# Optimization experiments

Measured on AMD Instinct MI355X. Metric: run time of the kernel, lower is better.

Reference implementation:

```python
import jax, jax.numpy as jnp
import numpy as np

N, E, MUL, ATTR, NBASIS = 30000, 480000, 32, 8, 8
AVG_NEIGH = 16.0
INV_SQRT3 = 1.0 / np.sqrt(3.0).astype(np.float32)  # wigner 3j (1,1,0)
LOG2 = float(np.log(2.0))


def ssp(x):
    # shifted softplus: softplus(x) - log(2)
    return jax.nn.softplus(x) - LOG2


def setup_inputs() -> dict:
    key = jax.random.key(0)
    ks = jax.random.split(key, 15)
    return {
        "node_s": jax.random.normal(ks[0], (N, MUL), jnp.float32),
        "node_v": jax.random.normal(ks[1], (N, MUL, 3), jnp.float32),
        "node_attr": jax.random.uniform(ks[2], (N, ATTR), jnp.float32),
        "edge_attr": jax.random.normal(ks[3], (E, 4), jnp.float32),       # [sh0 | sh1(3)]
        "edge_scalars": jax.random.uniform(ks[4], (E, NBASIS), jnp.float32),
        "W1_0": jax.random.normal(ks[5], (MUL, MUL), jnp.float32),
        "W1_1": jax.random.normal(ks[6], (MUL, MUL), jnp.float32),
        "Wfc1": jax.random.normal(ks[7], (NBASIS, NBASIS), jnp.float32),
        "Wfc2": jax.random.normal(ks[8], (NBASIS, 4 * MUL), jnp.float32),
        "W2_0": jax.random.normal(ks[9], (2 * MUL, MUL), jnp.float32),
        "W2_1": jax.random.normal(ks[10], (2 * MUL, MUL), jnp.float32),
        "Wsc0": jax.random.normal(ks[11], (MUL, ATTR, MUL), jnp.float32),
        "Wsc1": jax.random.normal(ks[12], (MUL, ATTR, MUL), jnp.float32),
        "edge_src": jax.random.randint(ks[13], (E,), 0, N, jnp.int32),
        "edge_dst": jax.random.randint(ks[14], (E,), 0, N, jnp.int32),
    }


def reference(node_s, node_v, node_attr, edge_attr, edge_scalars,
              W1_0, W1_1, Wfc1, Wfc2, W2_0, W2_1, Wsc0, Wsc1,
              edge_src, edge_dst):
    n_nodes, mul = node_s.shape
    # --- fc: radial MLP -> per-edge TP weights (shared_weights=False) ---
    h = ssp(edge_scalars @ Wfc1 * (1.0 / np.sqrt(Wfc1.shape[0])))
    w = h @ Wfc2 * (1.0 / np.sqrt(Wfc2.shape[0]))                 # [E, 4*MUL]
    w00, w01, w10, w11 = jnp.split(w, 4, axis=1)                  # instruction order
    # --- lin1: per-irrep linear (fan-in normalized) ---
    inv_m = 1.0 / np.sqrt(mul)
    x0 = node_s @ W1_0 * inv_m                                    # [N, MUL]
    x1 = jnp.einsum('nud,uw->nwd', node_v, W1_1) * inv_m          # [N, MUL, 3]
    # --- gather destination-node features per edge ---
    x0d, x1d = x0[edge_dst], x1[edge_dst]
    sh0, sh1 = edge_attr[:, :1], edge_attr[:, 1:4]
    # --- uvu tensor product with per-edge weights ---
    s_a = w00 * x0d * sh0                                         # 0e x 0e -> 0e
    s_b = w11 * jnp.einsum('eud,ed->eu', x1d, sh1) * INV_SQRT3    # 1o x 1o -> 0e
    v_a = (w01 * x0d)[:, :, None] * sh1[:, None, :]               # 0e x 1o -> 1o
    v_b = w10[:, :, None] * x1d * sh0[:, :, None]                 # 1o x 0e -> 1o
    mid_s = jnp.concatenate([s_a, s_b], axis=1)                   # [E, 64]  (64x0e)
    mid_v = jnp.concatenate([v_a, v_b], axis=1)                   # [E, 64, 3] (64x1o)
    # --- scatter-sum over edge_src, normalized by sqrt(avg_num_neighbors) ---
    inv_nb = 1.0 / np.sqrt(AVG_NEIGH)
    agg_s = jax.ops.segment_sum(mid_s, edge_src, num_segments=n_nodes) * inv_nb
    agg_v = jax.ops.segment_sum(mid_v, edge_src, num_segments=n_nodes) * inv_nb
    # --- lin2 ---
    inv_2m = 1.0 / np.sqrt(2.0 * mul)
    out0 = agg_s @ W2_0 * inv_2m                                  # [N, MUL]
    out1 = jnp.einsum('nud,uw->nwd', agg_v, W2_1) * inv_2m        # [N, MUL, 3]
    # --- self-connection: fully-connected TP (attr is scalar 8x0e) ---
    sc_norm = 1.0 / np.sqrt(mul * node_attr.shape[1])
    sc0 = jnp.einsum('nu,nv,uvw->nw', node_s, node_attr, Wsc0) * sc_norm
    sc1 = jnp.einsum('nud,nv,uvw->nwd', node_v, node_attr, Wsc1) * sc_norm
    o0 = out0 + sc0
    o1 = out1 + sc1
    return jnp.concatenate([o0, o1.reshape(n_nodes, mul * 3)], axis=1)  # [N, 128]
```

## Files before the change

### kernel.cpp

```cpp
#include <hip/hip_runtime.h>
#include <math.h>

#define N_NODES 30000
#define N_EDGES 480000

typedef __attribute__((ext_vector_type(8))) short short8;
typedef __attribute__((ext_vector_type(4))) float f32x4;
typedef __attribute__((ext_vector_type(2))) float f32x2;

__device__ __forceinline__ unsigned short f2bf(float f) {
    unsigned u = __float_as_uint(f);
    u += 0x7fff + ((u >> 16) & 1);
    return (unsigned short)(u >> 16);
}
__device__ __forceinline__ float bfLO(unsigned v) { return __uint_as_float(v << 16); }
__device__ __forceinline__ float bfHI(unsigned v) { return __uint_as_float(v & 0xffff0000u); }
__device__ __forceinline__ unsigned packbf(float a, float b) {
    return (unsigned)f2bf(a) | ((unsigned)f2bf(b) << 16);
}
__device__ __forceinline__ unsigned ptk(float a, float b) {
    return (__float_as_uint(a) >> 16) | (__float_as_uint(b) & 0xffff0000u);
}

union U8 { short8 v; unsigned u[4]; };
union C4 { f32x4 v; float f[4]; };

__global__ __launch_bounds__(256) void k_pre(
    const float* __restrict__ node_s,
    const float* __restrict__ node_v,
    const float* __restrict__ W1_0,
    const float* __restrict__ W1_1,
    const float* __restrict__ Wsc0,
    const float* __restrict__ Wsc1,
    const float* __restrict__ W2_0,
    const float* __restrict__ W2_1,
    const int* __restrict__ edge_src,
    int* __restrict__ deg,
    unsigned short* __restrict__ xnode,
    unsigned* __restrict__ bsc0,
    unsigned* __restrict__ bsc1,
    unsigned* __restrict__ b20,
    unsigned* __restrict__ b21)
{
    __shared__ float sVT[16 * 100];
    __shared__ float sXo[16 * 140];
    int tid = threadIdx.x;

    if (blockIdx.x >= 1875) {
        int b = blockIdx.x - 1875;
        const float* Wm = (b == 0) ? Wsc0 : (b == 1) ? Wsc1 : (b == 2) ? W2_0 : W2_1;
        unsigned* dst = (b == 0) ? bsc0 : (b == 1) ? bsc1 : (b == 2) ? b20 : b21;
        float scale = (b < 2) ? 0.0625f : 0.03125f;
        int nu = (b < 2) ? 4096 : 1024;
        for (int idx = tid; idx < nu; idx += 256) {
            int jp = idx & 3;
            int lane = (idx >> 2) & 63;
            int ft = (idx >> 8) & 1;
            int kc = idx >> 9;
            int quad = lane >> 4, col = lane & 15;
            int k = kc * 32 + quad * 8 + jp * 2;
            int c = ft * 16 + col;
            dst[idx] = packbf(Wm[k * 32 + c] * scale, Wm[(k + 1) * 32 + c] * scale);
        }
        return;
    }

    atomicAdd(&deg[edge_src[blockIdx.x * 256 + tid]], 1);

    int nbase = blockIdx.x * 16;
    for (int i = tid; i < 1536; i += 256) {
        int nl = i / 96, r = i - nl * 96;
        int u = r / 3, d = r - u * 3;
        sVT[nl * 100 + d * 32 + u] = node_v[(size_t)nbase * 96 + i];
    }
    __syncthreads();

    int lane = tid & 63;
    int wv = tid >> 6;
    int col = lane & 15, quad = lane >> 4, m = lane & 15;

    const float* W1 = (wv == 0) ? W1_0 : W1_1;
    U8 bf0, bf1;
#pragma unroll
    for (int p = 0; p < 4; ++p) {
        int k = quad * 8 + 2 * p;
        bf0.u[p] = packbf(W1[k * 32 + col],      W1[(k + 1) * 32 + col]);
        bf1.u[p] = packbf(W1[k * 32 + col + 16], W1[(k + 1) * 32 + col + 16]);
    }

    U8 af;
    if (wv == 0) {
        const float* sp = node_s + (size_t)(nbase + m) * 32 + quad * 8;
        float4 a0 = *(const float4*)(sp);
        float4 a1 = *(const float4*)(sp + 4);
        af.u[0] = packbf(a0.x, a0.y); af.u[1] = packbf(a0.z, a0.w);
        af.u[2] = packbf(a1.x, a1.y); af.u[3] = packbf(a1.z, a1.w);
    } else {
        int R = 16 * (wv - 1) + m;
        int nl = R / 3, d = R - nl * 3;
        const float* vp = sVT + nl * 100 + d * 32 + quad * 8;
        af.u[0] = packbf(vp[0], vp[1]); af.u[1] = packbf(vp[2], vp[3]);
        af.u[2] = packbf(vp[4], vp[5]); af.u[3] = packbf(vp[6], vp[7]);
    }

    f32x4 acc0 = {0.f, 0.f, 0.f, 0.f};
    f32x4 acc1 = {0.f, 0.f, 0.f, 0.f};
    acc0 = __builtin_amdgcn_mfma_f32_16x16x32_bf16(af.v, bf0.v, acc0, 0, 0, 0);
    acc1 = __builtin_amdgcn_mfma_f32_16x16x32_bf16(af.v, bf1.v, acc1, 0, 0, 0);

    C4 c0, c1;
    c0.v = acc0; c1.v = acc1;
    if (wv == 0) {
#pragma unroll
        for (int r = 0; r < 4; ++r) {
            int nl = (quad << 2) + r;
            sXo[nl * 140 + col]      = c0.f[r];
            sXo[nl * 140 + col + 16] = c1.f[r];
        }
    } else {
#pragma unroll
        for (int r = 0; r < 4; ++r) {
            int R = 16 * (wv - 1) + (quad << 2) + r;
            int nl = R / 3, d = R - nl * 3;
            sXo[nl * 140 + (1 + d) * 34 + col]      = c0.f[r];
            sXo[nl * 140 + (1 + d) * 34 + col + 16] = c1.f[r];
        }
    }
    __syncthreads();

    const float inv_m = 0.1767766953f;
    for (int i = tid; i < 512; i += 256) {
        int nl = i >> 5, u = i & 31;
        const float* xp = sXo + nl * 140;
        uint2 pk;
        pk.x = packbf(xp[u] * inv_m,       xp[34 + u] * inv_m);
        pk.y = packbf(xp[68 + u] * inv_m,  xp[102 + u] * inv_m);
        *(uint2*)(xnode + (size_t)(nbase + nl) * 128 + u * 4) = pk;
    }
}

__global__ __launch_bounds__(1024) void scan_kernel(const int* __restrict__ deg,
                                                    int* __restrict__ offs,
                                                    int* __restrict__ cursor) {
    __shared__ int sdeg[N_NODES];
    __shared__ int wsum[16];
    int tid = threadIdx.x;
#pragma unroll
    for (int k = 0; k < 30; ++k) {
        int idx = k * 1024 + tid;
        if (idx < N_NODES) sdeg[idx] = deg[idx];
    }
    __syncthreads();
    int base = tid * 30;
    int s = 0;
    if (base < N_NODES) {
#pragma unroll
        for (int k = 0; k < 30; ++k) s += sdeg[base + k];
    }
    int lane = tid & 63, wid = tid >> 6;
    int inc = s;
#pragma unroll
    for (int d = 1; d < 64; d <<= 1) {
        int o = __shfl_up(inc, d, 64);
        if (lane >= d) inc += o;
    }
    if (lane == 63) wsum[wid] = inc;
    __syncthreads();
    if (tid < 16) {
        int v = wsum[tid];
        int t = v;
#pragma unroll
        for (int d = 1; d < 16; d <<= 1) {
            int o = __shfl_up(t, d, 64);
            if (tid >= d) t += o;
        }
        wsum[tid] = t - v;
    }
    __syncthreads();
    int run = inc - s + wsum[wid];
    if (base < N_NODES) {
#pragma unroll
        for (int k = 0; k < 30; ++k) {
            int n = base + k;
            int d = sdeg[n];
            sdeg[n] = run;
            run += d;
        }
    }
    __syncthreads();
#pragma unroll
    for (int k = 0; k < 30; ++k) {
        int idx = k * 1024 + tid;
        if (idx < N_NODES) {
            int v = sdeg[idx];
            offs[idx] = v;
            cursor[idx] = v;
        }
    }
    if (tid == 0) offs[N_NODES] = N_EDGES;
}

__global__ __launch_bounds__(256) void fill_kernel(
    const float* __restrict__ edge_attr,
    const float* __restrict__ edge_scalars,
    const float* __restrict__ Wfc1,
    const int* __restrict__ edge_src,
    const int* __restrict__ edge_dst,
    int* __restrict__ cursor,
    uint4* __restrict__ rec)
{
    __shared__ float sW[64];
    int tid = threadIdx.x;
    if (tid < 64) sW[tid] = Wfc1[tid];
    __syncthreads();

    int e = blockIdx.x * 256 + tid;
    float4 es0 = *(const float4*)(edge_scalars + (size_t)e * 8);
    float4 es1 = *(const float4*)(edge_scalars + (size_t)e * 8 + 4);
    float4 ea  = *(const float4*)(edge_attr + (size_t)e * 4);
    int src = edge_src[e];
    int dst = edge_dst[e];
    int pos = atomicAdd(&cursor[src], 1);

    const float inv8 = 0.3535533906f;
    float h[8];
#pragma unroll
    for (int i = 0; i < 8; ++i) {
        float acc = es0.x * sW[0 * 8 + i];
        acc = fmaf(es0.y, sW[1 * 8 + i], acc);
        acc = fmaf(es0.z, sW[2 * 8 + i], acc);
        acc = fmaf(es0.w, sW[3 * 8 + i], acc);
        acc = fmaf(es1.x, sW[4 * 8 + i], acc);
        acc = fmaf(es1.y, sW[5 * 8 + i], acc);
        acc = fmaf(es1.z, sW[6 * 8 + i], acc);
        acc = fmaf(es1.w, sW[7 * 8 + i], acc);
        acc *= inv8;
        float ax = fabsf(acc);
        float tt = __expf(-ax);
        h[i] = fmaxf(acc, 0.f) + __logf(1.f + tt) - 0.6931471806f;
    }
    uint4 r0, r1;
    r0.x = packbf(h[0], h[1]); r0.y = packbf(h[2], h[3]);
    r0.z = packbf(h[4], h[5]); r0.w = packbf(h[6], h[7]);
    r1.x = packbf(ea.x, ea.y); r1.y = packbf(ea.z, ea.w);
    r1.z = ((unsigned)dst) << 8;
    r1.w = 0;
    rec[2 * pos]     = r0;
    rec[2 * pos + 1] = r1;
}

struct GAcc {
    float sa, sb, va2, vb2;
    f32x2 va01, vb01;
};

__device__ __forceinline__ void gstep(
    uint4& RS0, uint4& RS1, uint2& XS, const uint4& RN1, uint2& XN,
    int& t, int cntH, int& pf, int L,
    const char* recc, const char* xbc,
    const f32x2* wfA, const f32x2* wfB, GAcc& g)
{
    float hv[8];
    hv[0] = bfLO(RS0.x); hv[1] = bfHI(RS0.x);
    hv[2] = bfLO(RS0.y); hv[3] = bfHI(RS0.y);
    hv[4] = bfLO(RS0.z); hv[5] = bfHI(RS0.z);
    hv[6] = bfLO(RS0.w); hv[7] = bfHI(RS0.w);
    float sh0  = bfLO(RS1.x), s1xe = bfHI(RS1.x);
    float s1ye = bfLO(RS1.y), s1ze = bfHI(RS1.y);
    float xv0 = bfLO(XS.x), xd0 = bfHI(XS.x);
    float xd1 = bfLO(XS.y), xd2 = bfHI(XS.y);
    bool ok = (t < cntH);

    RS0 = *(const uint4*)(recc + pf);
    RS1 = *(const uint4*)(recc + pf + 16);
    pf = min(pf + 64, L);
    XN = *(const uint2*)(xbc + RN1.z);

    f32x2 aA = {0.f, 0.f}, aB = {0.f, 0.f};
#pragma unroll
    for (int q = 0; q < 8; ++q) {
        f32x2 hh = {hv[q], hv[q]};
        aA = __builtin_elementwise_fma(hh, wfA[q], aA);
        aB = __builtin_elementwise_fma(hh, wfB[q], aB);
    }
    float a00 = ok ? aA.x : 0.f;
    float a01 = ok ? aA.y : 0.f;
    float a10 = ok ? aB.x : 0.f;
    float a11 = ok ? aB.y : 0.f;

    float dot = xd0 * s1xe + xd1 * s1ye + xd2 * s1ze;
    g.sa = fmaf(a00 * sh0, xv0, g.sa);
    g.sb = fmaf(a11, dot, g.sb);
    float w01x0 = a01 * xv0;
    float t10 = a10 * sh0;
    f32x2 wb = {w01x0, w01x0};
    f32x2 tb = {t10, t10};
    f32x2 s01 = {s1xe, s1ye};
    f32x2 xd01 = {xd0, xd1};
    g.va01 = __builtin_elementwise_fma(wb, s01, g.va01);
    g.vb01 = __builtin_elementwise_fma(tb, xd01, g.vb01);
    g.va2 = fmaf(w01x0, s1ze, g.va2);
    g.vb2 = fmaf(t10, xd2, g.vb2);
    ++t;
}

__global__ __launch_bounds__(256) void k_gather(
    const int* __restrict__ offs,
    const uint4* __restrict__ rec,
    const float* __restrict__ Wfc2,
    const unsigned short* __restrict__ xnode,
    unsigned short* __restrict__ agg)
{
    int tid = threadIdx.x;
    int lane = tid & 63;
    int u = lane & 31;
    int half = lane >> 5;
    int wv = tid >> 6;
    int node = blockIdx.x * 4 + wv;

    const float inv8 = 0.3535533906f;
    const float i8s3 = 0.3535533906f * 0.5773502692f;
    f32x2 wfA[8], wfB[8];
#pragma unroll
    for (int q = 0; q < 8; ++q) {
        const float* wp = Wfc2 + q * 128 + u;
        wfA[q].x = wp[0]  * inv8;
        wfA[q].y = wp[32] * inv8;
        wfB[q].x = wp[64] * inv8;
        wfB[q].y = wp[96] * i8s3;
    }

    int beg = offs[node], end = offs[node + 1];
    int cnt = end - beg;

    GAcc g;
    g.sa = 0.f; g.sb = 0.f; g.va2 = 0.f; g.vb2 = 0.f;
    g.va01 = (f32x2){0.f, 0.f};
    g.vb01 = (f32x2){0.f, 0.f};

    if (cnt > 0) {
        const char* recc = (const char*)rec;
        const char* xbc  = (const char*)xnode + u * 8;
        int T = (cnt + 1) >> 1;
        int cntH = (cnt + 1 - half) >> 1;
        int L = (end - 1) * 32;
        int b0 = (beg + half) * 32;

        uint4 r00, r01, r10, r11, r20, r21, r30, r31, r40, r41, r50, r51;
        uint2 x0, x1, x2, x3, x4, x5;
        x4.x = 0u; x4.y = 0u; x5.x = 0u; x5.y = 0u;
        int p;
        p = min(b0,       L); r00 = *(const uint4*)(recc + p); r01 = *(const uint4*)(recc + p + 16);
        p = min(b0 + 64,  L); r10 = *(const uint4*)(recc + p); r11 = *(const uint4*)(recc + p + 16);
        p = min(b0 + 128, L); r20 = *(const uint4*)(recc + p); r21 = *(const uint4*)(recc + p + 16);
        p = min(b0 + 192, L); r30 = *(const uint4*)(recc + p); r31 = *(const uint4*)(recc + p + 16);
        p = min(b0 + 256, L); r40 = *(const uint4*)(recc + p); r41 = *(const uint4*)(recc + p + 16);
        p = min(b0 + 320, L); r50 = *(const uint4*)(recc + p); r51 = *(const uint4*)(recc + p + 16);
        int pf = min(b0 + 384, L);
        x0 = *(const uint2*)(xbc + r01.z);
        x1 = *(const uint2*)(xbc + r11.z);
        x2 = *(const uint2*)(xbc + r21.z);
        x3 = *(const uint2*)(xbc + r31.z);

        int t = 0;
        int Tm = T - 5;
        while (t < Tm) {
            gstep(r00, r01, x0, r41, x4, t, cntH, pf, L, recc, xbc, wfA, wfB, g);
            gstep(r10, r11, x1, r51, x5, t, cntH, pf, L, recc, xbc, wfA, wfB, g);
            gstep(r20, r21, x2, r01, x0, t, cntH, pf, L, recc, xbc, wfA, wfB, g);
            gstep(r30, r31, x3, r11, x1, t, cntH, pf, L, recc, xbc, wfA, wfB, g);
            gstep(r40, r41, x4, r21, x2, t, cntH, pf, L, recc, xbc, wfA, wfB, g);
            gstep(r50, r51, x5, r31, x3, t, cntH, pf, L, recc, xbc, wfA, wfB, g);
        }
        if (t < T) gstep(r00, r01, x0, r41, x4, t, cntH, pf, L, recc, xbc, wfA, wfB, g);
        if (t < T) gstep(r10, r11, x1, r51, x5, t, cntH, pf, L, recc, xbc, wfA, wfB, g);
        if (t < T) gstep(r20, r21, x2, r01, x0, t, cntH, pf, L, recc, xbc, wfA, wfB, g);
        if (t < T) gstep(r30, r31, x3, r11, x1, t, cntH, pf, L, recc, xbc, wfA, wfB, g);
        if (t < T) gstep(r40, r41, x4, r21, x2, t, cntH, pf, L, recc, xbc, wfA, wfB, g);
    }

    g.sa      += __shfl_xor(g.sa, 32, 64);
    g.sb      += __shfl_xor(g.sb, 32, 64);
    g.va01.x  += __shfl_xor(g.va01.x, 32, 64);
    g.va01.y  += __shfl_xor(g.va01.y, 32, 64);
    g.vb01.x  += __shfl_xor(g.vb01.x, 32, 64);
    g.vb01.y  += __shfl_xor(g.vb01.y, 32, 64);
    g.va2     += __shfl_xor(g.va2, 32, 64);
    g.vb2     += __shfl_xor(g.vb2, 32, 64);

    unsigned short* ap = agg + (size_t)node * 256;
    if (half == 0) {
        ap[u]       = f2bf(g.sa);
        ap[32 + u]  = f2bf(g.sb);
        ap[64 + u]  = f2bf(g.va01.x);
        ap[96 + u]  = f2bf(g.vb01.x);
    } else {
        ap[128 + u] = f2bf(g.va01.y);
        ap[160 + u] = f2bf(g.vb01.y);
        ap[192 + u] = f2bf(g.va2);
        ap[224 + u] = f2bf(g.vb2);
    }
}

__global__ __launch_bounds__(256) void k_gemm(
    const unsigned short* agg,
    const float* __restrict__ node_s,
    const float* __restrict__ node_v,
    const float* __restrict__ node_attr,
    const unsigned* __restrict__ bsc0,
    const unsigned* __restrict__ bsc1,
    const unsigned* __restrict__ b20,
    const unsigned* __restrict__ b21,
    float* out)
{
    __shared__ float sS[16 * 33];
    __shared__ float sV[16 * 100];
    int tid = threadIdx.x;
    int lane = tid & 63;
    int wv = tid >> 6;
    int nbase = blockIdx.x * 16;

    for (int i = tid; i < 512; i += 256)
        sS[(i >> 5) * 33 + (i & 31)] = node_s[(size_t)nbase * 32 + i];
    for (int i = tid; i < 1536; i += 256)
        sV[(i / 96) * 100 + (i % 96)] = node_v[(size_t)nbase * 96 + i];

    int col = lane & 15;
    int quad = lane >> 4;
    int m = col;
    bool is_s = (wv == 0);
    int sub = wv - 1;

    const short* Bs = (const short*)(is_s ? bsc0 : bsc1);
    const short* B2 = (const short*)(is_s ? b20 : b21);

    int aBase, fbase, fstep, n_a;
    if (is_s) {
        aBase = m * 256;
        fbase = m * 33;
        fstep = 1;
        n_a = nbase + m;
    } else {
        int r16 = 16 * sub + m;
        int nl = r16 / 3;
        int dd = r16 - nl * 3;
        aBase = nl * 256 + 64 + 64 * dd;
        fbase = nl * 100 + dd;
        fstep = 3;
        n_a = nbase + nl;
    }

    const short* aggp = (const short*)agg + (size_t)nbase * 256 + aBase + quad * 8;
    short8 afW0 = *(const short8*)(aggp);
    short8 afW1 = *(const short8*)(aggp + 32);

    float4 A0 = *(const float4*)(node_attr + (size_t)n_a * 8);
    float4 A1 = *(const float4*)(node_attr + (size_t)n_a * 8 + 4);
    float aa0 = A0.x, aa1 = A0.y, aa2 = A0.z, aa3 = A0.w;
    float aa4 = A1.x, aa5 = A1.y, aa6 = A1.z, aa7 = A1.w;

    __syncthreads();

    f32x4 acc0 = {0.f, 0.f, 0.f, 0.f};
    f32x4 acc1 = {0.f, 0.f, 0.f, 0.f};

    {
        short8 bf0 = *(const short8*)(B2 + (0 * 64 + lane) * 8);
        short8 bf1 = *(const short8*)(B2 + (1 * 64 + lane) * 8);
        acc0 = __builtin_amdgcn_mfma_f32_16x16x32_bf16(afW0, bf0, acc0, 0, 0, 0);
        acc1 = __builtin_amdgcn_mfma_f32_16x16x32_bf16(afW0, bf1, acc1, 0, 0, 0);
        bf0 = *(const short8*)(B2 + (2 * 64 + lane) * 8);
        bf1 = *(const short8*)(B2 + (3 * 64 + lane) * 8);
        acc0 = __builtin_amdgcn_mfma_f32_16x16x32_bf16(afW1, bf0, acc0, 0, 0, 0);
        acc1 = __builtin_amdgcn_mfma_f32_16x16x32_bf16(afW1, bf1, acc1, 0, 0, 0);
    }

    const float* Sf = is_s ? sS : sV;
#pragma unroll
    for (int kc = 0; kc < 8; ++kc) {
        int uu = kc * 4 + quad;
        float f = Sf[fbase + uu * fstep];
        U8 af;
        af.u[0] = ptk(f * aa0, f * aa1);
        af.u[1] = ptk(f * aa2, f * aa3);
        af.u[2] = ptk(f * aa4, f * aa5);
        af.u[3] = ptk(f * aa6, f * aa7);
        short8 bf0 = *(const short8*)(Bs + ((kc * 2 + 0) * 64 + lane) * 8);
        short8 bf1 = *(const short8*)(Bs + ((kc * 2 + 1) * 64 + lane) * 8);
        acc0 = __builtin_amdgcn_mfma_f32_16x16x32_bf16(af.v, bf0, acc0, 0, 0, 0);
        acc1 = __builtin_amdgcn_mfma_f32_16x16x32_bf16(af.v, bf1, acc1, 0, 0, 0);
    }

    C4 c0, c1;
    c0.v = acc0; c1.v = acc1;
    if (is_s) {
#pragma unroll
        for (int r = 0; r < 4; ++r) {
            int n = nbase + (quad << 2) + r;
            out[(size_t)n * 128 + col]      = c0.f[r];
            out[(size_t)n * 128 + col + 16] = c1.f[r];
        }
    } else {
#pragma unroll
        for (int r = 0; r < 4; ++r) {
            int rl = 16 * sub + (quad << 2) + r;
            int nn = rl / 3;
            int dd = rl - nn * 3;
            int n = nbase + nn;
            out[(size_t)n * 128 + 32 + 3 * col + dd]        = c0.f[r];
            out[(size_t)n * 128 + 32 + 3 * (col + 16) + dd] = c1.f[r];
        }
    }
}

extern "C" void kernel_launch(void* const* d_in, const int* in_sizes, int n_in,
                              void* d_out, int out_size, void* d_ws, size_t ws_size,
                              hipStream_t stream) {
    const float* node_s       = (const float*)d_in[0];
    const float* node_v       = (const float*)d_in[1];
    const float* node_attr    = (const float*)d_in[2];
    const float* edge_attr    = (const float*)d_in[3];
    const float* edge_scalars = (const float*)d_in[4];
    const float* W1_0 = (const float*)d_in[5];
    const float* W1_1 = (const float*)d_in[6];
    const float* Wfc1 = (const float*)d_in[7];
    const float* Wfc2 = (const float*)d_in[8];
    const float* W2_0 = (const float*)d_in[9];
    const float* W2_1 = (const float*)d_in[10];
    const float* Wsc0 = (const float*)d_in[11];
    const float* Wsc1 = (const float*)d_in[12];
    const int* edge_src = (const int*)d_in[13];
    const int* edge_dst = (const int*)d_in[14];

    char* ws = (char*)d_ws;
    unsigned short* xnode = (unsigned short*)(ws);
    uint4* rec            = (uint4*)(ws + 7680000);
    int* deg    = (int*)(ws + 23040000);
    int* offs   = (int*)(ws + 23160000);
    int* cursor = (int*)(ws + 23280016);
    unsigned* bsc0 = (unsigned*)(ws + 23400064);
    unsigned* bsc1 = (unsigned*)(ws + 23416448);
    unsigned* b20  = (unsigned*)(ws + 23432832);
    unsigned* b21  = (unsigned*)(ws + 23436928);

    hipMemsetAsync(deg, 0, (size_t)N_NODES * sizeof(int), stream);
    k_pre<<<1879, 256, 0, stream>>>(node_s, node_v, W1_0, W1_1, Wsc0, Wsc1,
                                    W2_0, W2_1, edge_src, deg, xnode,
                                    bsc0, bsc1, b20, b21);
    scan_kernel<<<1, 1024, 0, stream>>>(deg, offs, cursor);
    fill_kernel<<<1875, 256, 0, stream>>>(edge_attr, edge_scalars, Wfc1,
                                          edge_src, edge_dst, cursor, rec);
    k_gather<<<7500, 256, 0, stream>>>(offs, rec, Wfc2, xnode,
                                       (unsigned short*)d_out);
    k_gemm<<<1875, 256, 0, stream>>>((const unsigned short*)d_out,
                                     node_s, node_v, node_attr,
                                     bsc0, bsc1, b20, b21, (float*)d_out);
}
```

Baseline: 236.2 us.

## Fuse gather and GEMM kernels, keeping aggregated features in shared memory

Merges the per-node edge gather kernel and the node GEMM kernel into one kernel. Each wave now gathers four nodes in sequence and writes the bf16 aggregates into padded shared memory instead of global memory, and the MFMA stage reads them from LDS. Wfc2 is staged through shared memory once per block. This removes a kernel launch and the global write and re-read of the aggregate buffer. In exchange there are 4x fewer blocks, each wave processes its nodes serially, and more LDS is used per block, which may lower occupancy and hurt latency hiding in the gather.

```diff
diff --git a/kernel.cpp b/kernel.cpp
--- a/kernel.cpp
+++ b/kernel.cpp
@@ -304,106 +304,11 @@
     ++t;
 }
 
-__global__ __launch_bounds__(256) void k_gather(
+__global__ __launch_bounds__(256) void k_main(
     const int* __restrict__ offs,
     const uint4* __restrict__ rec,
     const float* __restrict__ Wfc2,
     const unsigned short* __restrict__ xnode,
-    unsigned short* __restrict__ agg)
-{
-    int tid = threadIdx.x;
-    int lane = tid & 63;
-    int u = lane & 31;
-    int half = lane >> 5;
-    int wv = tid >> 6;
-    int node = blockIdx.x * 4 + wv;
-
-    const float inv8 = 0.3535533906f;
-    const float i8s3 = 0.3535533906f * 0.5773502692f;
-    f32x2 wfA[8], wfB[8];
-#pragma unroll
-    for (int q = 0; q < 8; ++q) {
-        const float* wp = Wfc2 + q * 128 + u;
-        wfA[q].x = wp[0]  * inv8;
-        wfA[q].y = wp[32] * inv8;
-        wfB[q].x = wp[64] * inv8;
-        wfB[q].y = wp[96] * i8s3;
-    }
-
-    int beg = offs[node], end = offs[node + 1];
-    int cnt = end - beg;
-
-    GAcc g;
-    g.sa = 0.f; g.sb = 0.f; g.va2 = 0.f; g.vb2 = 0.f;
-    g.va01 = (f32x2){0.f, 0.f};
-    g.vb01 = (f32x2){0.f, 0.f};
-
-    if (cnt > 0) {
-        const char* recc = (const char*)rec;
-        const char* xbc  = (const char*)xnode + u * 8;
-        int T = (cnt + 1) >> 1;
-        int cntH = (cnt + 1 - half) >> 1;
-        int L = (end - 1) * 32;
-        int b0 = (beg + half) * 32;
-
-        uint4 r00, r01, r10, r11, r20, r21, r30, r31, r40, r41, r50, r51;
-        uint2 x0, x1, x2, x3, x4, x5;
-        x4.x = 0u; x4.y = 0u; x5.x = 0u; x5.y = 0u;
-        int p;
-        p = min(b0,       L); r00 = *(const uint4*)(recc + p); r01 = *(const uint4*)(recc + p + 16);
-        p = min(b0 + 64,  L); r10 = *(const uint4*)(recc + p); r11 = *(const uint4*)(recc + p + 16);
-        p = min(b0 + 128, L); r20 = *(const uint4*)(recc + p); r21 = *(const uint4*)(recc + p + 16);
-        p = min(b0 + 192, L); r30 = *(const uint4*)(recc + p); r31 = *(const uint4*)(recc + p + 16);
-        p = min(b0 + 256, L); r40 = *(const uint4*)(recc + p); r41 = *(const uint4*)(recc + p + 16);
-        p = min(b0 + 320, L); r50 = *(const uint4*)(recc + p); r51 = *(const uint4*)(recc + p + 16);
-        int pf = min(b0 + 384, L);
-        x0 = *(const uint2*)(xbc + r01.z);
-        x1 = *(const uint2*)(xbc + r11.z);
-        x2 = *(const uint2*)(xbc + r21.z);
-        x3 = *(const uint2*)(xbc + r31.z);
-
-        int t = 0;
-        int Tm = T - 5;
-        while (t < Tm) {
-            gstep(r00, r01, x0, r41, x4, t, cntH, pf, L, recc, xbc, wfA, wfB, g);
-            gstep(r10, r11, x1, r51, x5, t, cntH, pf, L, recc, xbc, wfA, wfB, g);
-            gstep(r20, r21, x2, r01, x0, t, cntH, pf, L, recc, xbc, wfA, wfB, g);
-            gstep(r30, r31, x3, r11, x1, t, cntH, pf, L, recc, xbc, wfA, wfB, g);
-            gstep(r40, r41, x4, r21, x2, t, cntH, pf, L, recc, xbc, wfA, wfB, g);
-            gstep(r50, r51, x5, r31, x3, t, cntH, pf, L, recc, xbc, wfA, wfB, g);
-        }
-        if (t < T) gstep(r00, r01, x0, r41, x4, t, cntH, pf, L, recc, xbc, wfA, wfB, g);
-        if (t < T) gstep(r10, r11, x1, r51, x5, t, cntH, pf, L, recc, xbc, wfA, wfB, g);
-        if (t < T) gstep(r20, r21, x2, r01, x0, t, cntH, pf, L, recc, xbc, wfA, wfB, g);
-        if (t < T) gstep(r30, r31, x3, r11, x1, t, cntH, pf, L, recc, xbc, wfA, wfB, g);
-        if (t < T) gstep(r40, r41, x4, r21, x2, t, cntH, pf, L, recc, xbc, wfA, wfB, g);
-    }
-
-    g.sa      += __shfl_xor(g.sa, 32, 64);
-    g.sb      += __shfl_xor(g.sb, 32, 64);
-    g.va01.x  += __shfl_xor(g.va01.x, 32, 64);
-    g.va01.y  += __shfl_xor(g.va01.y, 32, 64);
-    g.vb01.x  += __shfl_xor(g.vb01.x, 32, 64);
-    g.vb01.y  += __shfl_xor(g.vb01.y, 32, 64);
-    g.va2     += __shfl_xor(g.va2, 32, 64);
-    g.vb2     += __shfl_xor(g.vb2, 32, 64);
-
-    unsigned short* ap = agg + (size_t)node * 256;
-    if (half == 0) {
-        ap[u]       = f2bf(g.sa);
-        ap[32 + u]  = f2bf(g.sb);
-        ap[64 + u]  = f2bf(g.va01.x);
-        ap[96 + u]  = f2bf(g.vb01.x);
-    } else {
-        ap[128 + u] = f2bf(g.va01.y);
-        ap[160 + u] = f2bf(g.vb01.y);
-        ap[192 + u] = f2bf(g.va2);
-        ap[224 + u] = f2bf(g.vb2);
-    }
-}
-
-__global__ __launch_bounds__(256) void k_gemm(
-    const unsigned short* agg,
     const float* __restrict__ node_s,
     const float* __restrict__ node_v,
     const float* __restrict__ node_attr,
@@ -411,19 +316,118 @@
     const unsigned* __restrict__ bsc1,
     const unsigned* __restrict__ b20,
     const unsigned* __restrict__ b21,
-    float* out)
+    float* __restrict__ out)
 {
+    __shared__ float sWf[1024];
     __shared__ float sS[16 * 33];
     __shared__ float sV[16 * 100];
+    __shared__ unsigned short sAgg[16 * 264];
     int tid = threadIdx.x;
-    int lane = tid & 63;
-    int wv = tid >> 6;
+
+    const float inv8 = 0.3535533906f;
+    const float inv_s3 = 0.5773502692f;
+    for (int i = tid; i < 1024; i += 256) {
+        float sc = ((i & 127) >= 96) ? inv8 * inv_s3 : inv8;
+        sWf[i] = Wfc2[i] * sc;
+    }
     int nbase = blockIdx.x * 16;
-
     for (int i = tid; i < 512; i += 256)
         sS[(i >> 5) * 33 + (i & 31)] = node_s[(size_t)nbase * 32 + i];
     for (int i = tid; i < 1536; i += 256)
         sV[(i / 96) * 100 + (i % 96)] = node_v[(size_t)nbase * 96 + i];
+    __syncthreads();
+
+    int lane = tid & 63;
+    int u = lane & 31;
+    int half = lane >> 5;
+    int wv = tid >> 6;
+
+    f32x2 wfA[8], wfB[8];
+#pragma unroll
+    for (int q = 0; q < 8; ++q) {
+        const float* wp = sWf + q * 128 + u;
+        wfA[q].x = wp[0];  wfA[q].y = wp[32];
+        wfB[q].x = wp[64]; wfB[q].y = wp[96];
+    }
+
+    int nfirst = nbase + wv * 4;
+    int beg = offs[nfirst];
+#pragma unroll 1
+    for (int j = 0; j < 4; ++j) {
+        int end = offs[nfirst + j + 1];
+        int cnt = end - beg;
+
+        GAcc g;
+        g.sa = 0.f; g.sb = 0.f; g.va2 = 0.f; g.vb2 = 0.f;
+        g.va01 = (f32x2){0.f, 0.f};
+        g.vb01 = (f32x2){0.f, 0.f};
+
+        if (cnt > 0) {
+            const char* recc = (const char*)rec;
+            const char* xbc  = (const char*)xnode + u * 8;
+            int T = (cnt + 1) >> 1;
+            int cntH = (cnt + 1 - half) >> 1;
+            int L = (end - 1) * 32;
+            int b0 = (beg + half) * 32;
+
+            uint4 r00, r01, r10, r11, r20, r21, r30, r31, r40, r41, r50, r51;
+            uint2 x0, x1, x2, x3, x4, x5;
+            x4.x = 0u; x4.y = 0u; x5.x = 0u; x5.y = 0u;
+            int p;
+            p = min(b0,       L); r00 = *(const uint4*)(recc + p); r01 = *(const uint4*)(recc + p + 16);
+            p = min(b0 + 64,  L); r10 = *(const uint4*)(recc + p); r11 = *(const uint4*)(recc + p + 16);
+            p = min(b0 + 128, L); r20 = *(const uint4*)(recc + p); r21 = *(const uint4*)(recc + p + 16);
+            p = min(b0 + 192, L); r30 = *(const uint4*)(recc + p); r31 = *(const uint4*)(recc + p + 16);
+            p = min(b0 + 256, L); r40 = *(const uint4*)(recc + p); r41 = *(const uint4*)(recc + p + 16);
+            p = min(b0 + 320, L); r50 = *(const uint4*)(recc + p); r51 = *(const uint4*)(recc + p + 16);
+            int pf = min(b0 + 384, L);
+            x0 = *(const uint2*)(xbc + r01.z);
+            x1 = *(const uint2*)(xbc + r11.z);
+            x2 = *(const uint2*)(xbc + r21.z);
+            x3 = *(const uint2*)(xbc + r31.z);
+
+            int t = 0;
+            int Tm = T - 5;
+            while (t < Tm) {
+                gstep(r00, r01, x0, r41, x4, t, cntH, pf, L, recc, xbc, wfA, wfB, g);
+                gstep(r10, r11, x1, r51, x5, t, cntH, pf, L, recc, xbc, wfA, wfB, g);
+                gstep(r20, r21, x2, r01, x0, t, cntH, pf, L, recc, xbc, wfA, wfB, g);
+                gstep(r30, r31, x3, r11, x1, t, cntH, pf, L, recc, xbc, wfA, wfB, g);
+                gstep(r40, r41, x4, r21, x2, t, cntH, pf, L, recc, xbc, wfA, wfB, g);
+                gstep(r50, r51, x5, r31, x3, t, cntH, pf, L, recc, xbc, wfA, wfB, g);
+            }
+            if (t < T) gstep(r00, r01, x0, r41, x4, t, cntH, pf, L, recc, xbc, wfA, wfB, g);
+            if (t < T) gstep(r10, r11, x1, r51, x5, t, cntH, pf, L, recc, xbc, wfA, wfB, g);
+            if (t < T) gstep(r20, r21, x2, r01, x0, t, cntH, pf, L, recc, xbc, wfA, wfB, g);
+            if (t < T) gstep(r30, r31, x3, r11, x1, t, cntH, pf, L, recc, xbc, wfA, wfB, g);
+            if (t < T) gstep(r40, r41, x4, r21, x2, t, cntH, pf, L, recc, xbc, wfA, wfB, g);
+        }
+
+        g.sa      += __shfl_xor(g.sa, 32, 64);
+        g.sb      += __shfl_xor(g.sb, 32, 64);
+        g.va01.x  += __shfl_xor(g.va01.x, 32, 64);
+        g.va01.y  += __shfl_xor(g.va01.y, 32, 64);
+        g.vb01.x  += __shfl_xor(g.vb01.x, 32, 64);
+        g.vb01.y  += __shfl_xor(g.vb01.y, 32, 64);
+        g.va2     += __shfl_xor(g.va2, 32, 64);
+        g.vb2     += __shfl_xor(g.vb2, 32, 64);
+
+        int nl = wv * 4 + j;
+        unsigned short* ap = sAgg + nl * 264;
+        if (half == 0) {
+            ap[u]       = f2bf(g.sa);
+            ap[32 + u]  = f2bf(g.sb);
+            ap[64 + u]  = f2bf(g.va01.x);
+            ap[96 + u]  = f2bf(g.vb01.x);
+        } else {
+            ap[128 + u] = f2bf(g.va01.y);
+            ap[160 + u] = f2bf(g.vb01.y);
+            ap[192 + u] = f2bf(g.va2);
+            ap[224 + u] = f2bf(g.vb2);
+        }
+        beg = end;
+    }
+    __syncthreads();
 
     int col = lane & 15;
     int quad = lane >> 4;
@@ -436,7 +440,7 @@
 
     int aBase, fbase, fstep, n_a;
     if (is_s) {
-        aBase = m * 256;
+        aBase = m * 264;
         fbase = m * 33;
         fstep = 1;
         n_a = nbase + m;
@@ -444,37 +448,27 @@
         int r16 = 16 * sub + m;
         int nl = r16 / 3;
         int dd = r16 - nl * 3;
-        aBase = nl * 256 + 64 + 64 * dd;
+        aBase = nl * 264 + 64 + 64 * dd;
         fbase = nl * 100 + dd;
         fstep = 3;
         n_a = nbase + nl;
     }
-
-    const short* aggp = (const short*)agg + (size_t)nbase * 256 + aBase + quad * 8;
-    short8 afW0 = *(const short8*)(aggp);
-    short8 afW1 = *(const short8*)(aggp + 32);
-
     float4 A0 = *(const float4*)(node_attr + (size_t)n_a * 8);
     float4 A1 = *(const float4*)(node_attr + (size_t)n_a * 8 + 4);
     float aa0 = A0.x, aa1 = A0.y, aa2 = A0.z, aa3 = A0.w;
     float aa4 = A1.x, aa5 = A1.y, aa6 = A1.z, aa7 = A1.w;
 
-    __syncthreads();
-
     f32x4 acc0 = {0.f, 0.f, 0.f, 0.f};
     f32x4 acc1 = {0.f, 0.f, 0.f, 0.f};
 
-    {
-        short8 bf0 = *(const short8*)(B2 + (0 * 64 + lane) * 8);
-        short8 bf1 = *(const short8*)(B2 + (1 * 64 + lane) * 8);
-        acc0 = __builtin_amdgcn_mfma_f32_16x16x32_bf16(afW0, bf0, acc0, 0, 0, 0);
-        acc1 = __builtin_amdgcn_mfma_f32_16x16x32_bf16(afW0, bf1, acc1, 0, 0, 0);
-        bf0 = *(const short8*)(B2 + (2 * 64 + lane) * 8);
-        bf1 = *(const short8*)(B2 + (3 * 64 + lane) * 8);
-        acc0 = __builtin_amdgcn_mfma_f32_16x16x32_bf16(afW1, bf0, acc0, 0, 0, 0);
-        acc1 = __builtin_amdgcn_mfma_f32_16x16x32_bf16(afW1, bf1, acc1, 0, 0, 0);
-    }
-
+#pragma unroll
+    for (int kc = 0; kc < 2; ++kc) {
+        short8 af = *(const short8*)((const short*)sAgg + aBase + kc * 32 + quad * 8);
+        short8 bf0 = *(const short8*)(B2 + ((kc * 2 + 0) * 64 + lane) * 8);
+        short8 bf1 = *(const short8*)(B2 + ((kc * 2 + 1) * 64 + lane) * 8);
+        acc0 = __builtin_amdgcn_mfma_f32_16x16x32_bf16(af, bf0, acc0, 0, 0, 0);
+        acc1 = __builtin_amdgcn_mfma_f32_16x16x32_bf16(af, bf1, acc1, 0, 0, 0);
+    }
     const float* Sf = is_s ? sS : sV;
 #pragma unroll
     for (int kc = 0; kc < 8; ++kc) {
@@ -550,9 +544,7 @@
     scan_kernel<<<1, 1024, 0, stream>>>(deg, offs, cursor);
     fill_kernel<<<1875, 256, 0, stream>>>(edge_attr, edge_scalars, Wfc1,
                                           edge_src, edge_dst, cursor, rec);
-    k_gather<<<7500, 256, 0, stream>>>(offs, rec, Wfc2, xnode,
-                                       (unsigned short*)d_out);
-    k_gemm<<<1875, 256, 0, stream>>>((const unsigned short*)d_out,
+    k_main<<<1875, 256, 0, stream>>>(offs, rec, Wfc2, xnode,
                                      node_s, node_v, node_attr,
                                      bsc0, bsc1, b20, b21, (float*)d_out);
 }
```

New measurement: 230.2 us. -2.5%, faster.
